# Kernel tuning notes

Hardware: AMD Instinct MI355X
Metric: run time of the kernel (lower is better)

The kernel has to match this reference:

```python
import jax, jax.numpy as jnp
import numpy as np

B, S, HID = 1, 2048, 4096
NH, NKV = 32, 8
HD = HID // NH          # 128
N_REP = NH // NKV       # 4
ROPE_THETA = 10000.0


def setup_inputs() -> dict:
    key = jax.random.key(0)
    ks = jax.random.split(key, 5)
    scale = 0.02
    x = jax.random.normal(ks[0], (B, S, HID), dtype=jnp.float32)
    Wq = jax.random.normal(ks[1], (HID, HID), dtype=jnp.float32) * scale
    Wk = jax.random.normal(ks[2], (NKV * HD, HID), dtype=jnp.float32) * scale
    Wv = jax.random.normal(ks[3], (NKV * HD, HID), dtype=jnp.float32) * scale
    Wo = jax.random.normal(ks[4], (HID, HID), dtype=jnp.float32) * scale
    position_ids = jnp.broadcast_to(jnp.arange(S, dtype=jnp.int32)[None, :], (B, S))
    return {"x": x, "Wq": Wq, "Wk": Wk, "Wv": Wv, "Wo": Wo, "position_ids": position_ids}


def _rope_cache(seq_len, dtype):
    inv_freq = 1.0 / (ROPE_THETA ** (jnp.arange(0, HD, 2, dtype=jnp.float32) / HD))
    t = jnp.arange(seq_len, dtype=jnp.float32)
    freqs = t[:, None] * inv_freq[None, :]            # [S, HD/2]
    emb = jnp.concatenate([freqs, freqs], axis=-1)    # [S, HD]
    return jnp.cos(emb).astype(dtype), jnp.sin(emb).astype(dtype)


def _rotate_half(x):
    x1, x2 = x[..., : HD // 2], x[..., HD // 2:]
    return jnp.concatenate([-x2, x1], axis=-1)


def reference(x, Wq, Wk, Wv, Wo, position_ids):
    b, s, _ = x.shape
    # projections (nn.Linear: x @ W.T)
    q = (x @ Wq.T).reshape(b, s, NH, HD).transpose(0, 2, 1, 3)    # [B,NH,S,HD]
    k = (x @ Wk.T).reshape(b, s, NKV, HD).transpose(0, 2, 1, 3)   # [B,NKV,S,HD]
    v = (x @ Wv.T).reshape(b, s, NKV, HD).transpose(0, 2, 1, 3)
    # RoPE
    cos_c, sin_c = _rope_cache(s, x.dtype)
    cos = cos_c[position_ids][:, None, :, :]   # [B,1,S,HD]
    sin = sin_c[position_ids][:, None, :, :]
    q = q * cos + _rotate_half(q) * sin
    k = k * cos + _rotate_half(k) * sin
    # GQA repeat_kv
    k = jnp.repeat(k, N_REP, axis=1)   # [B,NH,S,HD]
    v = jnp.repeat(v, N_REP, axis=1)
    # scaled dot-product attention with causal mask
    scores = jnp.einsum('bhqd,bhkd->bhqk', q, k) / jnp.sqrt(jnp.float32(HD))
    causal = jnp.tril(jnp.ones((s, s), dtype=bool))
    scores = jnp.where(causal[None, None, :, :], scores, jnp.finfo(scores.dtype).min)
    attn = jax.nn.softmax(scores.astype(jnp.float32), axis=-1).astype(q.dtype)
    out = jnp.einsum('bhqk,bhkd->bhqd', attn, v)                  # [B,NH,S,HD]
    out = out.transpose(0, 2, 1, 3).reshape(b, s, NH * HD)
    return out @ Wo.T
```

## Files before the change

### kernel.cpp

```cpp
#include <hip/hip_runtime.h>
#include <hip/hip_bf16.h>

#define DEVI __device__ __forceinline__

typedef __attribute__((ext_vector_type(8))) __bf16 bf16x8;
typedef __attribute__((ext_vector_type(4))) float f32x4;

DEVI f32x4 mfma_16x16x32(bf16x8 a, bf16x8 b, f32x4 c) {
  return __builtin_amdgcn_mfma_f32_16x16x32_bf16(a, b, c, 0, 0, 0);
}

DEVI void gld16(const void* g, void* l) {
  __builtin_amdgcn_global_load_lds(
      reinterpret_cast<const __attribute__((address_space(1))) unsigned int*>(
          reinterpret_cast<unsigned long long>(g)),
      reinterpret_cast<__attribute__((address_space(3))) unsigned int*>(
          reinterpret_cast<unsigned long long>(l)),
      16, 0, 0);
}

DEVI unsigned short f2bf(float f) {
  unsigned u = __builtin_bit_cast(unsigned, f);
  u += 0x7FFFu + ((u >> 16) & 1u);
  return (unsigned short)(u >> 16);
}
DEVI float bf2f(unsigned short b) {
  return __builtin_bit_cast(float, (unsigned)b << 16);
}

struct Conv5 {
  const float4 *x, *wq, *wk, *wv, *wo;
  ushort4 *xb, *wqkv, *wob;
};
__global__ void k_conv_all(Conv5 a) {
  constexpr int C0 = 2097152;
  constexpr int C1 = C0 + 4194304;
  constexpr int C2 = C1 + 1048576;
  constexpr int C3 = C2 + 1048576;
  constexpr int C4 = C3 + 4194304;
  int stride = gridDim.x * blockDim.x;
  for (int i = blockIdx.x * blockDim.x + threadIdx.x; i < C4; i += stride) {
    const float4* src; ushort4* dst; int j;
    if (i < C0)      { src = a.x;  dst = a.xb;             j = i; }
    else if (i < C1) { src = a.wq; dst = a.wqkv;           j = i - C0; }
    else if (i < C2) { src = a.wk; dst = a.wqkv + 4194304; j = i - C1; }
    else if (i < C3) { src = a.wv; dst = a.wqkv + 5242880; j = i - C2; }
    else             { src = a.wo; dst = a.wob;            j = i - C3; }
    float4 v = src[j];
    ushort4 o; o.x = f2bf(v.x); o.y = f2bf(v.y); o.z = f2bf(v.z); o.w = f2bf(v.w);
    dst[j] = o;
  }
}

__global__ void k_rope_table(float2* __restrict__ tab) {
  int idx = blockIdx.x * blockDim.x + threadIdx.x;
  int s = idx >> 6, d = idx & 63;
  float invf = powf(10000.0f, -(float)d * (1.0f / 64.0f));
  float f = (float)s * invf;
  tab[idx] = make_float2(cosf(f), sinf(f));
}

template <int NH_, int L2NH>
__global__ void k_rope_v(unsigned short* __restrict__ X, const float2* __restrict__ tab,
                         const int* __restrict__ pos, float scale) {
  int t = blockIdx.x * blockDim.x + threadIdx.x;
  int d0 = (t & 7) * 8;
  int sh = t >> 3;
  int s  = sh >> L2NH;
  int h  = sh & (NH_ - 1);
  size_t base = (size_t)s * (NH_ * 128) + h * 128 + d0;
  const float4* tf = (const float4*)(tab + (size_t)pos[s] * 64 + d0);
  unsigned short a[8], b[8], oa[8], ob[8];
  *(ushort4*)&a[0] = *(const ushort4*)(X + base);
  *(ushort4*)&a[4] = *(const ushort4*)(X + base + 4);
  *(ushort4*)&b[0] = *(const ushort4*)(X + base + 64);
  *(ushort4*)&b[4] = *(const ushort4*)(X + base + 68);
#pragma unroll
  for (int j = 0; j < 4; ++j) {
    float4 cs = tf[j];
    float x1 = bf2f(a[2*j]),   x2 = bf2f(b[2*j]);
    float y1 = bf2f(a[2*j+1]), y2 = bf2f(b[2*j+1]);
    oa[2*j]   = f2bf((x1 * cs.x - x2 * cs.y) * scale);
    ob[2*j]   = f2bf((x2 * cs.x + x1 * cs.y) * scale);
    oa[2*j+1] = f2bf((y1 * cs.z - y2 * cs.w) * scale);
    ob[2*j+1] = f2bf((y2 * cs.z + y1 * cs.w) * scale);
  }
  *(ushort4*)(X + base)      = *(ushort4*)&oa[0];
  *(ushort4*)(X + base + 4)  = *(ushort4*)&oa[4];
  *(ushort4*)(X + base + 64) = *(ushort4*)&ob[0];
  *(ushort4*)(X + base + 68) = *(ushort4*)&ob[4];
}

template <int EPI>
__global__ __launch_bounds__(256, 2)
void k_gemm64(const unsigned short* __restrict__ A,
              const unsigned short* __restrict__ B,
              void* __restrict__ Cp,
              unsigned short* __restrict__ Kp,
              unsigned short* __restrict__ Vtp,
              int K) {
  __shared__ __align__(16) unsigned short As[128][64];
  __shared__ __align__(16) unsigned short Bs[128][64];
  const int tid  = threadIdx.x;
  const int lane = tid & 63;
  const int wave = tid >> 6;
  const int bm = blockIdx.y * 128;
  const int bn = blockIdx.x * 128;
  const int wm = (wave >> 1) * 64;
  const int wn = (wave & 1) * 64;
  const int l15 = lane & 15;
  const int lg  = lane >> 4;

  f32x4 acc[4][4] = {};

  const int srow  = lane >> 3;
  const int scol  = ((lane & 7) ^ srow) * 8;
  const unsigned short* aS = A + (size_t)(bm + wave * 32 + srow) * K + scol;
  const unsigned short* bS = B + (size_t)(bn + wave * 32 + srow) * K + scol;

  for (int k0 = 0; k0 < K; k0 += 64) {
    __syncthreads();
#pragma unroll
    for (int c = 0; c < 4; ++c) {
      gld16(aS + (size_t)(c * 8) * K + k0, &As[wave * 32 + c * 8][0]);
      gld16(bS + (size_t)(c * 8) * K + k0, &Bs[wave * 32 + c * 8][0]);
    }
    __syncthreads();

#pragma unroll
    for (int ks = 0; ks < 2; ++ks) {
      bf16x8 a[4], b[4];
#pragma unroll
      for (int m = 0; m < 4; ++m)
        a[m] = *(const bf16x8*)&As[wm + m * 16 + l15][((ks * 4 + lg) ^ (l15 & 7)) * 8];
#pragma unroll
      for (int n = 0; n < 4; ++n)
        b[n] = *(const bf16x8*)&Bs[wn + n * 16 + l15][((ks * 4 + lg) ^ (l15 & 7)) * 8];
#pragma unroll
      for (int m = 0; m < 4; ++m)
#pragma unroll
        for (int n = 0; n < 4; ++n)
          acc[m][n] = mfma_16x16x32(a[m], b[n], acc[m][n]);
    }
  }

#pragma unroll
  for (int m = 0; m < 4; ++m)
#pragma unroll
    for (int n = 0; n < 4; ++n)
#pragma unroll
      for (int r = 0; r < 4; ++r) {
        int row = bm + wm + m * 16 + lg * 4 + r;
        int col = bn + wn + n * 16 + l15;
        float v = acc[m][n][r];
        if (EPI == 0) {
          if (col < 4096)      ((unsigned short*)Cp)[(size_t)row * 4096 + col] = f2bf(v);
          else if (col < 5120) Kp[(size_t)row * 1024 + (col - 4096)] = f2bf(v);
          else                 Vtp[(size_t)(col - 5120) * 2048 + row] = f2bf(v);
        } else {
          ((float*)Cp)[(size_t)row * 4096 + col] = v;
        }
      }
}

__global__ __launch_bounds__(256, 2)
void k_attn(const unsigned short* __restrict__ Q,
            const unsigned short* __restrict__ Kb,
            const unsigned short* __restrict__ Vt,
            unsigned short* __restrict__ AO) {
  __shared__ __align__(16) unsigned short Kl[2][64][128];
  __shared__ __align__(16) unsigned short Vl[2][128][64];
  __shared__ __align__(16) unsigned short Pl[4][2][16][64];
  const int tid = threadIdx.x, lane = tid & 63, w = tid >> 6;
  const int bid = blockIdx.x;
  const int qi = 15 - (bid >> 5);
  const int h  = bid & 31;
  const int q0 = qi * 128;
  const int kh = h >> 2;
  const int l15 = lane & 15, lg = lane >> 4;
  const int swz = (l15 & 7);

  bf16x8 qf0[4], qf1[4];
  {
    const unsigned short* qr0 = Q + (size_t)(q0 + w * 16 + l15) * 4096 + h * 128;
    const unsigned short* qr1 = qr0 + (size_t)64 * 4096;
#pragma unroll
    for (int ks = 0; ks < 4; ++ks) {
      qf0[ks] = *(const bf16x8*)(qr0 + ks * 32 + lg * 8);
      qf1[ks] = *(const bf16x8*)(qr1 + ks * 32 + lg * 8);
    }
  }

  f32x4 o0[8] = {}, o1[8] = {};
  float m0 = -1e30f, l0 = 0.f, m1 = -1e30f, l1 = 0.f;
  const int nkb  = 2 * qi + 2;
  const int myq0 = q0 + w * 16 + l15;
  const int myq1 = myq0 + 64;

  auto stageK = [&](int buf, int kv0) {
#pragma unroll
    for (int c = 0; c < 4; ++c) {
      int row = 16 * w + 4 * c + lg;
      gld16(Kb + (size_t)(kv0 + row) * 1024 + kh * 128 + ((l15 ^ (row & 7)) * 8),
            &Kl[buf][16 * w + 4 * c][0]);
    }
  };
  auto stageV = [&](int buf, int kv0) {
#pragma unroll
    for (int c = 0; c < 4; ++c) {
      int row = 32 * w + 8 * c + (lane >> 3);
      gld16(Vt + (size_t)(kh * 128 + row) * 2048 + kv0 + (((lane & 7) ^ (row & 7)) * 8),
            &Vl[buf][32 * w + 8 * c][0]);
    }
  };

  stageK(0, 0);
  stageV(0, 0);
  int cur = 0;

  for (int kb = 0; kb < nkb; ++kb) {
    const int kv0 = kb * 64;
    __syncthreads();
    if (kb + 1 < nkb) { stageK(cur ^ 1, kv0 + 64); stageV(cur ^ 1, kv0 + 64); }

    const bool skip0 = (kb == nkb - 1);
    const bool maskt = (kb >= nkb - 2);

    f32x4 s0[4] = {}, s1[4] = {};
    __builtin_amdgcn_s_setprio(1);
#pragma unroll
    for (int ks = 0; ks < 4; ++ks)
#pragma unroll
      for (int n = 0; n < 4; ++n) {
        bf16x8 bk = *(const bf16x8*)&Kl[cur][n * 16 + l15][((ks * 4 + lg) ^ swz) * 8];
        if (!skip0) s0[n] = mfma_16x16x32(bk, qf0[ks], s0[n]);
        s1[n] = mfma_16x16x32(bk, qf1[ks], s1[n]);
      }
    __builtin_amdgcn_s_setprio(0);

    if (maskt) {
#pragma unroll
      for (int n = 0; n < 4; ++n)
#pragma unroll
        for (int r = 0; r < 4; ++r) {
          int kv = kv0 + n * 16 + lg * 4 + r;
          if (!skip0 && kv > myq0) s0[n][r] = -1e30f;
          if (kv > myq1)           s1[n][r] = -1e30f;
        }
    }

    if (!skip0) {
      float mx = -1e30f;
#pragma unroll
      for (int n = 0; n < 4; ++n)
        mx = fmaxf(mx, fmaxf(fmaxf(s0[n][0], s0[n][1]), fmaxf(s0[n][2], s0[n][3])));
      mx = fmaxf(mx, __shfl_xor(mx, 16));
      mx = fmaxf(mx, __shfl_xor(mx, 32));
      if (!__all(mx <= m0 + 8.0f)) {
        float mn = fmaxf(m0, mx);
        float fac = __expf(m0 - mn);
        m0 = mn; l0 *= fac;
#pragma unroll
        for (int j = 0; j < 8; ++j) {
          o0[j][0] *= fac; o0[j][1] *= fac; o0[j][2] *= fac; o0[j][3] *= fac;
        }
      }
      float rs = 0.f;
#pragma unroll
      for (int n = 0; n < 4; ++n)
#pragma unroll
        for (int r = 0; r < 4; ++r) {
          float pv = __expf(s0[n][r] - m0);
          s0[n][r] = pv; rs += pv;
        }
      rs += __shfl_xor(rs, 16);
      rs += __shfl_xor(rs, 32);
      l0 += rs;
#pragma unroll
      for (int n = 0; n < 4; ++n) {
        ushort4 pk;
        pk.x = f2bf(s0[n][0]); pk.y = f2bf(s0[n][1]);
        pk.z = f2bf(s0[n][2]); pk.w = f2bf(s0[n][3]);
        *(ushort4*)&Pl[w][0][l15][(((2 * n + (lg >> 1)) ^ swz) << 3) + ((lg & 1) << 2)] = pk;
      }
    }
    {
      float mx = -1e30f;
#pragma unroll
      for (int n = 0; n < 4; ++n)
        mx = fmaxf(mx, fmaxf(fmaxf(s1[n][0], s1[n][1]), fmaxf(s1[n][2], s1[n][3])));
      mx = fmaxf(mx, __shfl_xor(mx, 16));
      mx = fmaxf(mx, __shfl_xor(mx, 32));
      if (!__all(mx <= m1 + 8.0f)) {
        float mn = fmaxf(m1, mx);
        float fac = __expf(m1 - mn);
        m1 = mn; l1 *= fac;
#pragma unroll
        for (int j = 0; j < 8; ++j) {
          o1[j][0] *= fac; o1[j][1] *= fac; o1[j][2] *= fac; o1[j][3] *= fac;
        }
      }
      float rs = 0.f;
#pragma unroll
      for (int n = 0; n < 4; ++n)
#pragma unroll
        for (int r = 0; r < 4; ++r) {
          float pv = __expf(s1[n][r] - m1);
          s1[n][r] = pv; rs += pv;
        }
      rs += __shfl_xor(rs, 16);
      rs += __shfl_xor(rs, 32);
      l1 += rs;
#pragma unroll
      for (int n = 0; n < 4; ++n) {
        ushort4 pk;
        pk.x = f2bf(s1[n][0]); pk.y = f2bf(s1[n][1]);
        pk.z = f2bf(s1[n][2]); pk.w = f2bf(s1[n][3]);
        *(ushort4*)&Pl[w][1][l15][(((2 * n + (lg >> 1)) ^ swz) << 3) + ((lg & 1) << 2)] = pk;
      }
    }
    asm volatile("s_waitcnt lgkmcnt(0)" ::: "memory");

    bf16x8 pa00, pa01;
    if (!skip0) {
      pa00 = *(const bf16x8*)&Pl[w][0][l15][(lg ^ swz) << 3];
      pa01 = *(const bf16x8*)&Pl[w][0][l15][((4 + lg) ^ swz) << 3];
    }
    bf16x8 pa10 = *(const bf16x8*)&Pl[w][1][l15][(lg ^ swz) << 3];
    bf16x8 pa11 = *(const bf16x8*)&Pl[w][1][l15][((4 + lg) ^ swz) << 3];

    __builtin_amdgcn_s_setprio(1);
#pragma unroll
    for (int j = 0; j < 8; ++j) {
      bf16x8 bv0 = *(const bf16x8*)&Vl[cur][j * 16 + l15][(lg ^ swz) * 8];
      bf16x8 bv1 = *(const bf16x8*)&Vl[cur][j * 16 + l15][((4 + lg) ^ swz) * 8];
      if (!skip0) {
        o0[j] = mfma_16x16x32(bv0, pa00, o0[j]);
        o0[j] = mfma_16x16x32(bv1, pa01, o0[j]);
      }
      o1[j] = mfma_16x16x32(bv0, pa10, o1[j]);
      o1[j] = mfma_16x16x32(bv1, pa11, o1[j]);
    }
    __builtin_amdgcn_s_setprio(0);
    cur ^= 1;
  }

  float inv0 = 1.0f / l0, inv1 = 1.0f / l1;
  __syncthreads();
  unsigned short* O0 = &Kl[0][0][0];
  unsigned short* O1 = &Vl[0][0][0];
#pragma unroll
  for (int j = 0; j < 8; ++j) {
    ushort4 t0, t1;
    t0.x = f2bf(o0[j][0] * inv0); t0.y = f2bf(o0[j][1] * inv0);
    t0.z = f2bf(o0[j][2] * inv0); t0.w = f2bf(o0[j][3] * inv0);
    t1.x = f2bf(o1[j][0] * inv1); t1.y = f2bf(o1[j][1] * inv1);
    t1.z = f2bf(o1[j][2] * inv1); t1.w = f2bf(o1[j][3] * inv1);
    *(ushort4*)&O0[w * 2176 + l15 * 136 + j * 16 + lg * 4] = t0;
    *(ushort4*)&O1[w * 2176 + l15 * 136 + j * 16 + lg * 4] = t1;
  }
  asm volatile("s_waitcnt lgkmcnt(0)" ::: "memory");
#pragma unroll
  for (int p = 0; p < 4; ++p) {
    int row = p * 4 + lg;
    bf16x8 v0 = *(const bf16x8*)&O0[w * 2176 + row * 136 + l15 * 8];
    bf16x8 v1 = *(const bf16x8*)&O1[w * 2176 + row * 136 + l15 * 8];
    *(bf16x8*)(AO + (size_t)(q0 + w * 16 + row) * 4096 + h * 128 + l15 * 8) = v0;
    *(bf16x8*)(AO + (size_t)(q0 + 64 + w * 16 + row) * 4096 + h * 128 + l15 * 8) = v1;
  }
}

extern "C" void kernel_launch(void* const* d_in, const int* in_sizes, int n_in,
                              void* d_out, int out_size, void* d_ws, size_t ws_size,
                              hipStream_t stream) {
  const float* x  = (const float*)d_in[0];
  const float* Wq = (const float*)d_in[1];
  const float* Wk = (const float*)d_in[2];
  const float* Wv = (const float*)d_in[3];
  const float* Wo = (const float*)d_in[4];
  const int*   pos = (const int*)d_in[5];
  float* out = (float*)d_out;

  char* p = (char*)d_ws;
  unsigned short* xb   = (unsigned short*)p; p += (size_t)2048 * 4096 * 2;
  unsigned short* wqkv = (unsigned short*)p; p += (size_t)6144 * 4096 * 2;
  unsigned short* wob  = (unsigned short*)p; p += (size_t)4096 * 4096 * 2;
  unsigned short* qb   = (unsigned short*)p; p += (size_t)2048 * 4096 * 2;
  unsigned short* kb   = (unsigned short*)p; p += (size_t)2048 * 1024 * 2;
  unsigned short* vtb  = (unsigned short*)p; p += (size_t)1024 * 2048 * 2;
  unsigned short* aob  = (unsigned short*)p; p += (size_t)2048 * 4096 * 2;
  float2*         tab  = (float2*)p;         p += (size_t)2048 * 64 * 8;

  Conv5 ca;
  ca.x  = (const float4*)x;  ca.wq = (const float4*)Wq; ca.wk = (const float4*)Wk;
  ca.wv = (const float4*)Wv; ca.wo = (const float4*)Wo;
  ca.xb = (ushort4*)xb; ca.wqkv = (ushort4*)wqkv; ca.wob = (ushort4*)wob;
  k_conv_all<<<4096, 256, 0, stream>>>(ca);
  k_rope_table<<<512, 256, 0, stream>>>(tab);

  k_gemm64<0><<<dim3(48, 16), 256, 0, stream>>>(xb, wqkv, qb, kb, vtb, 4096);

  const float scale = 0.08838834764831845f;
  k_rope_v<32, 5><<<2048, 256, 0, stream>>>(qb, tab, pos, scale);
  k_rope_v<8, 3><<<512, 256, 0, stream>>>(kb, tab, pos, 1.0f);

  k_attn<<<512, 256, 0, stream>>>(qb, kb, vtb, aob);

  k_gemm64<1><<<dim3(32, 16), 256, 0, stream>>>(aob, wob, out, nullptr, nullptr, 4096);
}
```

Measured before the change: 522.3 us.

## Pair low and high query tiles per attention block and use exp2 softmax

Each attention block now takes one 64-row query tile from the start and one from the end of the sequence, instead of two adjacent tiles. This evens out causal work across blocks, since every block now runs 33 key-tile iterations in total, and it removes load imbalance and tail effects. The softmax switches from __expf to exp2f, with log2(e) folded into the Q scale inside the RoPE kernel, and the rescale threshold is raised to match. The P-to-bf16 conversion now truncates instead of rounding to nearest, which saves a few integer ops per element at some cost in accuracy.

Result: faster. 510.1 us (-2.3%).

```diff
diff --git a/kernel.cpp b/kernel.cpp
--- a/kernel.cpp
+++ b/kernel.cpp
@@ -23,6 +23,9 @@
   unsigned u = __builtin_bit_cast(unsigned, f);
   u += 0x7FFFu + ((u >> 16) & 1u);
   return (unsigned short)(u >> 16);
+}
+DEVI unsigned short f2bf_trunc(float f) {
+  return (unsigned short)(__builtin_bit_cast(unsigned, f) >> 16);
 }
 DEVI float bf2f(unsigned short b) {
   return __builtin_bit_cast(float, (unsigned)b << 16);
@@ -173,17 +176,20 @@
   __shared__ __align__(16) unsigned short Pl[4][2][16][64];
   const int tid = threadIdx.x, lane = tid & 63, w = tid >> 6;
   const int bid = blockIdx.x;
-  const int qi = 15 - (bid >> 5);
+  const int qi = bid >> 5;
   const int h  = bid & 31;
-  const int q0 = qi * 128;
+  const int lq0 = qi * 64;
+  const int hq0 = (31 - qi) * 64;
+  const int lo_nkb = qi + 1;
+  const int hi_nkb = 32 - qi;
   const int kh = h >> 2;
   const int l15 = lane & 15, lg = lane >> 4;
   const int swz = (l15 & 7);
 
   bf16x8 qf0[4], qf1[4];
   {
-    const unsigned short* qr0 = Q + (size_t)(q0 + w * 16 + l15) * 4096 + h * 128;
-    const unsigned short* qr1 = qr0 + (size_t)64 * 4096;
+    const unsigned short* qr0 = Q + (size_t)(lq0 + w * 16 + l15) * 4096 + h * 128;
+    const unsigned short* qr1 = Q + (size_t)(hq0 + w * 16 + l15) * 4096 + h * 128;
 #pragma unroll
     for (int ks = 0; ks < 4; ++ks) {
       qf0[ks] = *(const bf16x8*)(qr0 + ks * 32 + lg * 8);
@@ -193,9 +199,8 @@
 
   f32x4 o0[8] = {}, o1[8] = {};
   float m0 = -1e30f, l0 = 0.f, m1 = -1e30f, l1 = 0.f;
-  const int nkb  = 2 * qi + 2;
-  const int myq0 = q0 + w * 16 + l15;
-  const int myq1 = myq0 + 64;
+  const int myq0 = lq0 + w * 16 + l15;
+  const int myq1 = hq0 + w * 16 + l15;
 
   auto stageK = [&](int buf, int kv0) {
 #pragma unroll
@@ -218,13 +223,14 @@
   stageV(0, 0);
   int cur = 0;
 
-  for (int kb = 0; kb < nkb; ++kb) {
+  for (int kb = 0; kb < hi_nkb; ++kb) {
     const int kv0 = kb * 64;
     __syncthreads();
-    if (kb + 1 < nkb) { stageK(cur ^ 1, kv0 + 64); stageV(cur ^ 1, kv0 + 64); }
-
-    const bool skip0 = (kb == nkb - 1);
-    const bool maskt = (kb >= nkb - 2);
+    if (kb + 1 < hi_nkb) { stageK(cur ^ 1, kv0 + 64); stageV(cur ^ 1, kv0 + 64); }
+
+    const bool act0  = (kb < lo_nkb);
+    const bool mask0 = (kb == lo_nkb - 1);
+    const bool mask1 = (kb == hi_nkb - 1);
 
     f32x4 s0[4] = {}, s1[4] = {};
     __builtin_amdgcn_s_setprio(1);
@@ -233,32 +239,36 @@
 #pragma unroll
       for (int n = 0; n < 4; ++n) {
         bf16x8 bk = *(const bf16x8*)&Kl[cur][n * 16 + l15][((ks * 4 + lg) ^ swz) * 8];
-        if (!skip0) s0[n] = mfma_16x16x32(bk, qf0[ks], s0[n]);
+        if (act0) s0[n] = mfma_16x16x32(bk, qf0[ks], s0[n]);
         s1[n] = mfma_16x16x32(bk, qf1[ks], s1[n]);
       }
     __builtin_amdgcn_s_setprio(0);
 
-    if (maskt) {
-#pragma unroll
-      for (int n = 0; n < 4; ++n)
-#pragma unroll
-        for (int r = 0; r < 4; ++r) {
-          int kv = kv0 + n * 16 + lg * 4 + r;
-          if (!skip0 && kv > myq0) s0[n][r] = -1e30f;
-          if (kv > myq1)           s1[n][r] = -1e30f;
-        }
-    }
-
-    if (!skip0) {
+    if (mask0) {
+#pragma unroll
+      for (int n = 0; n < 4; ++n)
+#pragma unroll
+        for (int r = 0; r < 4; ++r)
+          if (kv0 + n * 16 + lg * 4 + r > myq0) s0[n][r] = -1e30f;
+    }
+    if (mask1) {
+#pragma unroll
+      for (int n = 0; n < 4; ++n)
+#pragma unroll
+        for (int r = 0; r < 4; ++r)
+          if (kv0 + n * 16 + lg * 4 + r > myq1) s1[n][r] = -1e30f;
+    }
+
+    if (act0) {
       float mx = -1e30f;
 #pragma unroll
       for (int n = 0; n < 4; ++n)
         mx = fmaxf(mx, fmaxf(fmaxf(s0[n][0], s0[n][1]), fmaxf(s0[n][2], s0[n][3])));
       mx = fmaxf(mx, __shfl_xor(mx, 16));
       mx = fmaxf(mx, __shfl_xor(mx, 32));
-      if (!__all(mx <= m0 + 8.0f)) {
+      if (!__all(mx <= m0 + 11.5f)) {
         float mn = fmaxf(m0, mx);
-        float fac = __expf(m0 - mn);
+        float fac = exp2f(m0 - mn);
         m0 = mn; l0 *= fac;
 #pragma unroll
         for (int j = 0; j < 8; ++j) {
@@ -270,7 +280,7 @@
       for (int n = 0; n < 4; ++n)
 #pragma unroll
         for (int r = 0; r < 4; ++r) {
-          float pv = __expf(s0[n][r] - m0);
+          float pv = exp2f(s0[n][r] - m0);
           s0[n][r] = pv; rs += pv;
         }
       rs += __shfl_xor(rs, 16);
@@ -279,8 +289,8 @@
 #pragma unroll
       for (int n = 0; n < 4; ++n) {
         ushort4 pk;
-        pk.x = f2bf(s0[n][0]); pk.y = f2bf(s0[n][1]);
-        pk.z = f2bf(s0[n][2]); pk.w = f2bf(s0[n][3]);
+        pk.x = f2bf_trunc(s0[n][0]); pk.y = f2bf_trunc(s0[n][1]);
+        pk.z = f2bf_trunc(s0[n][2]); pk.w = f2bf_trunc(s0[n][3]);
         *(ushort4*)&Pl[w][0][l15][(((2 * n + (lg >> 1)) ^ swz) << 3) + ((lg & 1) << 2)] = pk;
       }
     }
@@ -291,9 +301,9 @@
         mx = fmaxf(mx, fmaxf(fmaxf(s1[n][0], s1[n][1]), fmaxf(s1[n][2], s1[n][3])));
       mx = fmaxf(mx, __shfl_xor(mx, 16));
       mx = fmaxf(mx, __shfl_xor(mx, 32));
-      if (!__all(mx <= m1 + 8.0f)) {
+      if (!__all(mx <= m1 + 11.5f)) {
         float mn = fmaxf(m1, mx);
-        float fac = __expf(m1 - mn);
+        float fac = exp2f(m1 - mn);
         m1 = mn; l1 *= fac;
 #pragma unroll
         for (int j = 0; j < 8; ++j) {
@@ -305,7 +315,7 @@
       for (int n = 0; n < 4; ++n)
 #pragma unroll
         for (int r = 0; r < 4; ++r) {
-          float pv = __expf(s1[n][r] - m1);
+          float pv = exp2f(s1[n][r] - m1);
           s1[n][r] = pv; rs += pv;
         }
       rs += __shfl_xor(rs, 16);
@@ -314,15 +324,15 @@
 #pragma unroll
       for (int n = 0; n < 4; ++n) {
         ushort4 pk;
-        pk.x = f2bf(s1[n][0]); pk.y = f2bf(s1[n][1]);
-        pk.z = f2bf(s1[n][2]); pk.w = f2bf(s1[n][3]);
+        pk.x = f2bf_trunc(s1[n][0]); pk.y = f2bf_trunc(s1[n][1]);
+        pk.z = f2bf_trunc(s1[n][2]); pk.w = f2bf_trunc(s1[n][3]);
         *(ushort4*)&Pl[w][1][l15][(((2 * n + (lg >> 1)) ^ swz) << 3) + ((lg & 1) << 2)] = pk;
       }
     }
     asm volatile("s_waitcnt lgkmcnt(0)" ::: "memory");
 
     bf16x8 pa00, pa01;
-    if (!skip0) {
+    if (act0) {
       pa00 = *(const bf16x8*)&Pl[w][0][l15][(lg ^ swz) << 3];
       pa01 = *(const bf16x8*)&Pl[w][0][l15][((4 + lg) ^ swz) << 3];
     }
@@ -334,7 +344,7 @@
     for (int j = 0; j < 8; ++j) {
       bf16x8 bv0 = *(const bf16x8*)&Vl[cur][j * 16 + l15][(lg ^ swz) * 8];
       bf16x8 bv1 = *(const bf16x8*)&Vl[cur][j * 16 + l15][((4 + lg) ^ swz) * 8];
-      if (!skip0) {
+      if (act0) {
         o0[j] = mfma_16x16x32(bv0, pa00, o0[j]);
         o0[j] = mfma_16x16x32(bv1, pa01, o0[j]);
       }
@@ -365,8 +375,8 @@
     int row = p * 4 + lg;
     bf16x8 v0 = *(const bf16x8*)&O0[w * 2176 + row * 136 + l15 * 8];
     bf16x8 v1 = *(const bf16x8*)&O1[w * 2176 + row * 136 + l15 * 8];
-    *(bf16x8*)(AO + (size_t)(q0 + w * 16 + row) * 4096 + h * 128 + l15 * 8) = v0;
-    *(bf16x8*)(AO + (size_t)(q0 + 64 + w * 16 + row) * 4096 + h * 128 + l15 * 8) = v1;
+    *(bf16x8*)(AO + (size_t)(lq0 + w * 16 + row) * 4096 + h * 128 + l15 * 8) = v0;
+    *(bf16x8*)(AO + (size_t)(hq0 + w * 16 + row) * 4096 + h * 128 + l15 * 8) = v1;
   }
 }
 
@@ -400,8 +410,8 @@
 
   k_gemm64<0><<<dim3(48, 16), 256, 0, stream>>>(xb, wqkv, qb, kb, vtb, 4096);
 
-  const float scale = 0.08838834764831845f;
-  k_rope_v<32, 5><<<2048, 256, 0, stream>>>(qb, tab, pos, scale);
+  const float scale2 = 0.08838834764831845f * 1.4426950408889634f;
+  k_rope_v<32, 5><<<2048, 256, 0, stream>>>(qb, tab, pos, scale2);
   k_rope_v<8, 3><<<512, 256, 0, stream>>>(kb, tab, pos, 1.0f);
 
   k_attn<<<512, 256, 0, stream>>>(qb, kb, vtb, aob);
```
